# Optimization experiments

Hardware: AMD Instinct MI355X
Metric: run time of the kernel (lower is better)

Reference implementation:

```python
import jax, jax.numpy as jnp
import numpy as np

B, N, C_IN, C_OUT = 2, 512, 64, 64  # mid_dim == out_dim
EPS = 1e-5

def _bn(x, g, b):
    # PyTorch BatchNorm1d in training mode: biased batch stats over axis 0 of [M, C]
    mu = x.mean(axis=0)
    var = x.var(axis=0)
    return (x - mu) * jax.lax.rsqrt(var + EPS) * g + b

def setup_inputs() -> dict:
    key = jax.random.key(0)
    ks = jax.random.split(key, 16)
    s = 0.05
    return {
        "pos": jax.random.normal(ks[0], (B, N, 3), jnp.float32),
        "c_features": jax.random.normal(ks[1], (B, N, C_IN), jnp.float32),
        "Wq": jax.random.normal(ks[2], (C_OUT, C_IN), jnp.float32) * s,
        "bq": jnp.zeros((C_OUT,), jnp.float32),
        "Wk": jax.random.normal(ks[3], (C_OUT, C_IN), jnp.float32) * s,
        "bk": jnp.zeros((C_OUT,), jnp.float32),
        "Wv": jax.random.normal(ks[4], (C_OUT, C_IN), jnp.float32) * s,
        "bv": jnp.zeros((C_OUT,), jnp.float32),
        "Wp1": jax.random.normal(ks[5], (3, 3), jnp.float32) * s,
        "bp1": jnp.zeros((3,), jnp.float32),
        "g_p": jnp.ones((3,), jnp.float32),
        "b_p": jnp.zeros((3,), jnp.float32),
        "Wp2": jax.random.normal(ks[6], (C_OUT, 3), jnp.float32) * s,
        "bp2": jnp.zeros((C_OUT,), jnp.float32),
        "g_w": jnp.ones((C_OUT,), jnp.float32),
        "b_w": jnp.zeros((C_OUT,), jnp.float32),
        "Ww1": jax.random.normal(ks[7], (C_OUT, C_OUT), jnp.float32) * s,
        "bw1": jnp.zeros((C_OUT,), jnp.float32),
        "Ww2": jax.random.normal(ks[8], (C_OUT, C_OUT), jnp.float32) * s,
        "bw2": jnp.zeros((C_OUT,), jnp.float32),
    }

def reference(pos, c_features, Wq, bq, Wk, bk, Wv, bv, Wp1, bp1, g_p, b_p, Wp2, bp2, g_w, b_w, Ww1, bw1, Ww2, bw2):
    b, n = pos.shape[0], pos.shape[1]
    q = c_features @ Wq.T + bq                       # [B,N,Cmid]
    k = c_features @ Wk.T + bk
    v = c_features @ Wv.T + bv                       # [B,N,Cout]
    rel = pos[:, :, None, :] - pos[:, None, :, :]    # [B,N,N,3]
    h = rel.reshape(-1, 3) @ Wp1.T + bp1             # [B*N*N,3]
    h = jax.nn.relu(_bn(h, g_p, b_p))
    delta = (h @ Wp2.T + bp2).reshape(b, n, n, -1)   # [B,N,N,Cmid]
    qk = q[:, :, None, :] - k[:, None, :, :] + delta # [B,N,N,Cmid]
    h2 = _bn(qk.reshape(-1, qk.shape[-1]), g_w, b_w)
    h2 = jax.nn.relu(h2)
    h2 = jax.nn.relu(h2 @ Ww1.T + bw1)
    w = (h2 @ Ww2.T + bw2).reshape(b, n, n, -1)      # [B,N,N,Cout]
    attn = jax.nn.softmax(w, axis=2)                 # softmax over j
    out = jnp.sum(attn * (v[:, None, :, :] + delta), axis=2)  # [B,N,Cout]
    return out
```

## Files before the change

### kernel.cpp

```cpp
#include <hip/hip_runtime.h>
#include <stdint.h>
#include <stddef.h>

#define DEV __device__ __forceinline__

typedef __attribute__((ext_vector_type(4))) float f32x4;
typedef __attribute__((ext_vector_type(8))) short bf16x8;

union FragU { bf16x8 f; uint32_t u[4]; };

DEV uint32_t pk_bf16(float a, float b) {
  uint32_t d;
  asm("v_cvt_pk_bf16_f32 %0, %1, %2" : "=v"(d) : "v"(a), "v"(b));
  return d;
}

DEV uint16_t f2bf(float x) {
  uint32_t u = __float_as_uint(x);
  u += 0x7fffu + ((u >> 16) & 1u);
  return (uint16_t)(u >> 16);
}

__launch_bounds__(256)
__global__ void kP(const float* __restrict__ cf, const float* __restrict__ pos,
                   const float* __restrict__ Wq, const float* __restrict__ Wk,
                   const float* __restrict__ Wv, const float* __restrict__ bq,
                   const float* __restrict__ bk, const float* __restrict__ bv,
                   const float* __restrict__ Ww1, const float* __restrict__ Ww2,
                   const float* __restrict__ Wp1, const float* __restrict__ g_p,
                   const float* __restrict__ bp2,
                   float* __restrict__ qo, float* __restrict__ ko,
                   float* __restrict__ vT, uint16_t* __restrict__ W1bf,
                   uint16_t* __restrict__ W2bf, float* __restrict__ a1out,
                   unsigned int* __restrict__ counter) {
  const int bid = blockIdx.x, t = threadIdx.x;
  if (bid < 256) {
    __shared__ float cfl[4][64];
    const int rr = t >> 6, c = t & 63;
    const int r0 = bid * 4;
    cfl[rr][c] = cf[(size_t)(r0 + rr) * 64 + c];
    __syncthreads();
    const int bn = r0 + rr;
    const float* wqr = Wq + c * 64;
    const float* wkr = Wk + c * 64;
    const float* wvr = Wv + c * 64;
    float aq = bq[c], ak = bk[c], av = bv[c] + bp2[c];
#pragma unroll 8
    for (int kk = 0; kk < 64; ++kk) {
      const float f = cfl[rr][kk];
      aq = fmaf(f, wqr[kk], aq);
      ak = fmaf(f, wkr[kk], ak);
      av = fmaf(f, wvr[kk], av);
    }
    qo[(size_t)bn * 64 + c] = aq;
    ko[(size_t)bn * 64 + c] = ak;
    vT[((size_t)(bn >> 9) * 64 + c) * 512 + (bn & 511)] = av;
  } else if (bid == 256) {
    const float L2E = 1.4426950408889634f;
    for (int idx = t; idx < 8192; idx += 256) {
      const int m = idx >> 12;
      const int r = idx & 4095;
      const int f = r >> 9;
      const int l = (r >> 3) & 63;
      const int e = r & 7;
      const int nt = f >> 1, ks = f & 1, lm = l & 15, lq = l >> 4;
      const int row = 16 * nt + lm, col = 8 * lq + 32 * ks + e;
      const float src = m ? (Ww2[row * 64 + col] * L2E) : Ww1[row * 64 + col];
      (m ? W2bf : W1bf)[r] = f2bf(src);
    }
  } else {
    if (t == 0) counter[0] = 0u;
    __shared__ float acc9[2][9];
    __shared__ float red[256][10];
    __shared__ float red2[9][16];
    for (int b = 0; b < 2; ++b) {
      float s[9];
#pragma unroll
      for (int a = 0; a < 9; ++a) s[a] = 0.f;
      for (int r = 0; r < 2; ++r) {
        int i = t + 256 * r;
        const float* p = pos + (size_t)(b * 512 + i) * 3;
        float p0 = p[0], p1 = p[1], p2 = p[2];
        s[0] += p0; s[1] += p1; s[2] += p2;
        s[3] += p0 * p0; s[4] += p0 * p1; s[5] += p0 * p2;
        s[6] += p1 * p1; s[7] += p1 * p2; s[8] += p2 * p2;
      }
#pragma unroll
      for (int a = 0; a < 9; ++a) red[t][a] = s[a];
      __syncthreads();
      if (t < 144) {
        const int a = t >> 4, p = t & 15;
        float v = 0.f;
#pragma unroll
        for (int qq = 0; qq < 16; ++qq) v += red[p * 16 + qq][a];
        red2[a][p] = v;
      }
      __syncthreads();
      if (t < 9) {
        float v = 0.f;
#pragma unroll
        for (int p = 0; p < 16; ++p) v += red2[t][p];
        acc9[b][t] = v;
      }
      __syncthreads();
    }
    if (t == 0) {
      float C[6] = {0.f, 0.f, 0.f, 0.f, 0.f, 0.f};
      const float invM = 1.0f / 524288.0f;
      for (int b = 0; b < 2; ++b) {
        float S0 = acc9[b][0], S1 = acc9[b][1], S2 = acc9[b][2];
        float G00 = acc9[b][3], G01 = acc9[b][4], G02 = acc9[b][5];
        float G11 = acc9[b][6], G12 = acc9[b][7], G22 = acc9[b][8];
        C[0] += 1024.f * G00 - 2.f * S0 * S0;
        C[1] += 1024.f * G01 - 2.f * S0 * S1;
        C[2] += 1024.f * G02 - 2.f * S0 * S2;
        C[3] += 1024.f * G11 - 2.f * S1 * S1;
        C[4] += 1024.f * G12 - 2.f * S1 * S2;
        C[5] += 1024.f * G22 - 2.f * S2 * S2;
      }
      for (int a = 0; a < 6; ++a) C[a] *= invM;
      for (int tt = 0; tt < 3; ++tt) {
        float w0 = Wp1[tt * 3 + 0], w1 = Wp1[tt * 3 + 1], w2 = Wp1[tt * 3 + 2];
        float var = w0 * w0 * C[0] + w1 * w1 * C[3] + w2 * w2 * C[5]
                  + 2.f * (w0 * w1 * C[1] + w0 * w2 * C[2] + w1 * w2 * C[4]);
        a1out[tt] = g_p[tt] * rsqrtf(var + 1e-5f);
      }
      a1out[3] = 0.f;
    }
  }
}

__launch_bounds__(256)
__global__ void kB(const float* __restrict__ pos, const float* __restrict__ a1,
                   const float* __restrict__ Wp1, const float* __restrict__ b_p,
                   const float* __restrict__ q, const float* __restrict__ k,
                   const float* __restrict__ bp2,
                   const float* __restrict__ g_w, const float* __restrict__ b_w,
                   const float* __restrict__ Wp2,
                   float* __restrict__ hpa, float* __restrict__ Mpart,
                   float* __restrict__ XPp, float* __restrict__ SNp,
                   unsigned int* __restrict__ counter,
                   float* __restrict__ a2o, float* __restrict__ be2o,
                   float* __restrict__ PtT) {
  const int bid = blockIdx.x, t = threadIdx.x;
  const int s = bid >> 4, b = (bid >> 3) & 1, chunk = bid & 7;

  __shared__ __align__(16) f32x4 X[512];
  __shared__ float U[64][64];
  __shared__ float redr[64][4][4];
  __shared__ float mred[256][6];
  __shared__ float mred2[64][6];
  __shared__ float rfin[64][4];
  __shared__ float redn[256][2];
  __shared__ float MfS[6];
  __shared__ float ShfS[3];
  __shared__ unsigned int isLast;

  {
    const float a10 = a1[0], a11 = a1[1], a12 = a1[2];
    const float w00 = Wp1[0], w01 = Wp1[1], w02 = Wp1[2];
    const float w10 = Wp1[3], w11 = Wp1[4], w12 = Wp1[5];
    const float w20 = Wp1[6], w21 = Wp1[7], w22 = Wp1[8];
    for (int r = 0; r < 2; ++r) {
      const int row = t + 256 * r;
      const float* p = pos + (size_t)(b * 512 + row) * 3;
      const float p0 = p[0], p1 = p[1], p2 = p[2];
      f32x4 v;
      v.x = a10 * (w00 * p0 + w01 * p1 + w02 * p2);
      v.y = a11 * (w10 * p0 + w11 * p1 + w12 * p2);
      v.z = a12 * (w20 * p0 + w21 * p1 + w22 * p2);
      v.w = 0.f;
      if (s == 0 && chunk == 0)
        *(f32x4*)(hpa + (size_t)(b * 512 + row) * 4) = v;
      if (s) { v.x = -v.x; v.y = -v.y; v.z = -v.z; }
      X[row] = v;
    }
  }
  {
    const float* src = s ? k : q;
    const int r0g = b * 512 + chunk * 64;
#pragma unroll
    for (int e = 0; e < 16; ++e) {
      const int idx = e * 256 + t;
      const int row = idx >> 6, c = idx & 63;
      float v = src[(size_t)(r0g + row) * 64 + c];
      if (!s) v += bp2[c];
      U[row][c] = v;
    }
  }
  __syncthreads();

  {
    const int al = t >> 2, qr = t & 3;
    const int a = chunk * 64 + al;
    const f32x4 xa = X[a];
    const float base0 = xa.x + b_p[0], base1 = xa.y + b_p[1], base2 = xa.z + b_p[2];
    float r0 = 0, r1 = 0, r2 = 0;
    float m00 = 0, m01 = 0, m02 = 0, m11 = 0, m12 = 0, m22 = 0;
#pragma unroll 8
    for (int jj = qr * 128; jj < qr * 128 + 128; ++jj) {
      const f32x4 xj = X[jj];
      const float h0 = fmaxf(0.f, base0 - xj.x);
      const float h1 = fmaxf(0.f, base1 - xj.y);
      const float h2 = fmaxf(0.f, base2 - xj.z);
      r0 += h0; r1 += h1; r2 += h2;
      if (s == 0) {
        m00 = fmaf(h0, h0, m00); m01 = fmaf(h0, h1, m01); m02 = fmaf(h0, h2, m02);
        m11 = fmaf(h1, h1, m11); m12 = fmaf(h1, h2, m12); m22 = fmaf(h2, h2, m22);
      }
    }
    redr[al][qr][0] = r0; redr[al][qr][1] = r1; redr[al][qr][2] = r2; redr[al][qr][3] = 0.f;
    mred[t][0] = m00; mred[t][1] = m01; mred[t][2] = m02;
    mred[t][3] = m11; mred[t][4] = m12; mred[t][5] = m22;
  }
  __syncthreads();

  if (t < 64) {
    float sx = 0, sy = 0, sz = 0;
#pragma unroll
    for (int p = 0; p < 4; ++p) { sx += redr[t][p][0]; sy += redr[t][p][1]; sz += redr[t][p][2]; }
    rfin[t][0] = sx; rfin[t][1] = sy; rfin[t][2] = sz; rfin[t][3] = 0.f;
    if (s == 0) {
#pragma unroll
      for (int cc = 0; cc < 6; ++cc)
        mred2[t][cc] = mred[t][cc] + mred[t + 64][cc] + mred[t + 128][cc] + mred[t + 192][cc];
    }
  }
  __syncthreads();

  if (s == 0 && t < 6) {
    float m = 0.f;
    for (int p = 0; p < 64; ++p) m += mred2[p][t];
    Mpart[bid * 12 + t] = m;
  }
  if (s == 0 && t >= 64 && t < 67) {
    const int tt = t - 64;
    float v = 0.f;
#pragma unroll 8
    for (int a = 0; a < 64; ++a) v += rfin[a][tt];
    Mpart[bid * 12 + 6 + tt] = v;
  }
  if (t < 192) {
    const int c = t & 63, tt = t >> 6;
    float xp = 0.f;
#pragma unroll 8
    for (int a = 0; a < 64; ++a) xp = fmaf(U[a][c], rfin[a][tt], xp);
    if (s) xp = -xp;
    XPp[((size_t)bid * 3 + tt) * 64 + c] = xp;
  }
  {
    const int c = t & 63, g = t >> 6;
    float su = 0.f, su2 = 0.f;
#pragma unroll
    for (int r = 0; r < 16; ++r) {
      const float v = U[g * 16 + r][c];
      su += v;
      su2 = fmaf(v, v, su2);
    }
    redn[t][0] = su; redn[t][1] = su2;
  }
  __syncthreads();
  if (t < 64) {
    float a0 = 0.f, a1v = 0.f;
#pragma unroll
    for (int p = 0; p < 4; ++p) { a0 += redn[t + 64 * p][0]; a1v += redn[t + 64 * p][1]; }
    SNp[((size_t)bid * 2 + 0) * 64 + t] = a0;
    SNp[((size_t)bid * 2 + 1) * 64 + t] = a1v;
  }

  __syncthreads();
  if (t == 0) {
    __threadfence();
    const unsigned int old = atomicAdd(counter, 1u);
    isLast = (old == 31u) ? 1u : 0u;
  }
  __syncthreads();
  if (isLast) {
    __threadfence();
    if (t < 6) {
      float m = 0.f;
#pragma unroll
      for (int p = 0; p < 16; ++p) m += Mpart[p * 12 + t];
      MfS[t] = m;
    }
    if (t >= 6 && t < 9) {
      const int tt = t - 6;
      float v = 0.f;
#pragma unroll
      for (int p = 0; p < 16; ++p) v += Mpart[p * 12 + 6 + tt];
      ShfS[tt] = v;
    }
    __syncthreads();
    if (t < 64) {
      const int c = t;
      float Su[2], Su2[2], Sk[2], Sk2[2];
#pragma unroll
      for (int bb = 0; bb < 2; ++bb) {
        float a0 = 0.f, a1v = 0.f, a2v = 0.f, a3 = 0.f;
#pragma unroll
        for (int p = 0; p < 8; ++p) {
          const int blkU = bb * 8 + p;
          const int blkK = 16 + bb * 8 + p;
          a0 += SNp[((size_t)blkU * 2 + 0) * 64 + c];
          a1v += SNp[((size_t)blkU * 2 + 1) * 64 + c];
          a2v += SNp[((size_t)blkK * 2 + 0) * 64 + c];
          a3 += SNp[((size_t)blkK * 2 + 1) * 64 + c];
        }
        Su[bb] = a0; Su2[bb] = a1v; Sk[bb] = a2v; Sk2[bb] = a3;
      }
      float URd0 = 0.f, URd1 = 0.f, URd2 = 0.f;
#pragma unroll
      for (int blk = 0; blk < 32; ++blk) {
        URd0 += XPp[((size_t)blk * 3 + 0) * 64 + c];
        URd1 += XPp[((size_t)blk * 3 + 1) * 64 + c];
        URd2 += XPp[((size_t)blk * 3 + 2) * 64 + c];
      }
      const float P0t = Wp2[c * 3 + 0], P1t = Wp2[c * 3 + 1], P2t = Wp2[c * 3 + 2];
      const float Nf = 512.f, invM = 1.f / 524288.f;
      float S1 = 0.f, Q2 = 0.f;
#pragma unroll
      for (int bb = 0; bb < 2; ++bb) {
        S1 += Nf * (Su[bb] - Sk[bb]);
        Q2 += Nf * Su2[bb] - 2.f * Su[bb] * Sk[bb] + Nf * Sk2[bb];
      }
      const float Xc = P0t * URd0 + P1t * URd1 + P2t * URd2;
      S1 += P0t * ShfS[0] + P1t * ShfS[1] + P2t * ShfS[2];
      const float Hm = P0t * P0t * MfS[0] + 2.f * P0t * P1t * MfS[1] + 2.f * P0t * P2t * MfS[2]
                     + P1t * P1t * MfS[3] + 2.f * P1t * P2t * MfS[4] + P2t * P2t * MfS[5];
      const float E1 = S1 * invM;
      const float E2 = (Q2 + 2.f * Xc + Hm) * invM;
      const float var = E2 - E1 * E1;
      const float rstd = rsqrtf(var + 1e-5f);
      const float A2 = g_w[c] * rstd;
      a2o[c] = A2;
      be2o[c] = b_w[c] - E1 * A2;
      PtT[0 * 64 + c] = A2 * P0t;
      PtT[1 * 64 + c] = A2 * P1t;
      PtT[2 * 64 + c] = A2 * P2t;
    }
  }
}

__launch_bounds__(256)
__global__ void k3_main(const float* __restrict__ q, const float* __restrict__ kk_,
                        const float* __restrict__ vT, const float* __restrict__ hpa,
                        const float* __restrict__ a2g, const float* __restrict__ be2g,
                        const float* __restrict__ PtTg,
                        const uint16_t* __restrict__ W1bf, const uint16_t* __restrict__ W2bf,
                        const float* __restrict__ bp2, const float* __restrict__ Wp2,
                        const float* __restrict__ b_p, const float* __restrict__ bw1g,
                        const float* __restrict__ bw2g, float* __restrict__ out) {
  const int bid = blockIdx.x;
  const int b = bid >> 9, i = bid & 511;
  const int t = threadIdx.x;
  const int wid = t >> 6, l = t & 63;
  const int lm = l & 15, lq = l >> 4;

  __shared__ __align__(16) uint16_t W1l[4096];
  __shared__ __align__(16) uint16_t W2l[4096];
  __shared__ __align__(16) uint16_t H2[4][16][76];
  __shared__ __align__(16) float P0[64];
  __shared__ __align__(16) float a2s[64];
  __shared__ __align__(16) float Pts[3][64];
  __shared__ __align__(16) float comb[4][64][2];

  {
    *(bf16x8*)(&W1l[t * 16])     = *(const bf16x8*)(W1bf + t * 16);
    *(bf16x8*)(&W1l[t * 16 + 8]) = *(const bf16x8*)(W1bf + t * 16 + 8);
    *(bf16x8*)(&W2l[t * 16])     = *(const bf16x8*)(W2bf + t * 16);
    *(bf16x8*)(&W2l[t * 16 + 8]) = *(const bf16x8*)(W2bf + t * 16 + 8);
  }
  if (t < 64) {
    const float a2v = a2g[t];
    a2s[t] = a2v;
    P0[t] = fmaf(a2v, q[(size_t)(b * 512 + i) * 64 + t] + bp2[t], be2g[t]);
  } else {
    const int idx = t - 64;
    Pts[idx >> 6][idx & 63] = PtTg[idx];
  }

  const f32x4 hi = *(const f32x4*)(hpa + (size_t)(b * 512 + i) * 4);
  const float bb0 = b_p[0], bb1 = b_p[1], bb2 = b_p[2];
  const float LOG2E = 1.4426950408889634f;

  float bw1r[4], bw2l[4], wpa[4], wpb[4], wpc[4];
#pragma unroll
  for (int nt = 0; nt < 4; ++nt) {
    const int c = 16 * nt + lm;
    bw1r[nt] = bw1g[c];
    bw2l[nt] = bw2g[c] * LOG2E;
    wpa[nt] = Wp2[c * 3 + 0];
    wpb[nt] = Wp2[c * 3 + 1];
    wpc[nt] = Wp2[c * 3 + 2];
  }

  float l_[4] = {0.f, 0.f, 0.f, 0.f};
  float acc_[4] = {0.f, 0.f, 0.f, 0.f};

  __syncthreads();

  const float* kbase = kk_ + (size_t)(b * 512) * 64;
  const float* hbase = hpa + (size_t)(b * 512) * 4;
  const float* vTb = vT + (size_t)b * 64 * 512;

  f32x4 kvA[2][2];
  {
    const int j0 = wid * 16 + lm;
#pragma unroll
    for (int ks = 0; ks < 2; ++ks) {
      kvA[ks][0] = *(const f32x4*)(kbase + (size_t)j0 * 64 + 32 * ks + 8 * lq);
      kvA[ks][1] = *(const f32x4*)(kbase + (size_t)j0 * 64 + 32 * ks + 8 * lq + 4);
    }
  }

  for (int it = 0; it < 8; ++it) {
    const int jb = it * 64 + wid * 16;
    const int j = jb + lm;
    const int j2 = jb + 4 * lq;

    f32x4 kvN[2][2];
    if (it < 7) {
      const int jn = j + 64;
#pragma unroll
      for (int ks = 0; ks < 2; ++ks) {
        kvN[ks][0] = *(const f32x4*)(kbase + (size_t)jn * 64 + 32 * ks + 8 * lq);
        kvN[ks][1] = *(const f32x4*)(kbase + (size_t)jn * 64 + 32 * ks + 8 * lq + 4);
      }
    }

    const f32x4 hj = *(const f32x4*)(hbase + j * 4);
    f32x4 hjr[4];
#pragma unroll
    for (int r = 0; r < 4; ++r) hjr[r] = *(const f32x4*)(hbase + (j2 + r) * 4);
    f32x4 vv[4];
#pragma unroll
    for (int nt = 0; nt < 4; ++nt)
      vv[nt] = *(const f32x4*)(vTb + (size_t)(16 * nt + lm) * 512 + j2);

    const float h0 = fmaxf(0.f, hi.x - hj.x + bb0);
    const float h1 = fmaxf(0.f, hi.y - hj.y + bb1);
    const float h2v = fmaxf(0.f, hi.z - hj.z + bb2);

    FragU A1[2];
#pragma unroll
    for (int ks = 0; ks < 2; ++ks) {
      const int c0 = 32 * ks + 8 * lq;
      f32x4 pv[2], av[2], t0[2], t1[2], t2[2];
      pv[0] = *(const f32x4*)(P0 + c0);        pv[1] = *(const f32x4*)(P0 + c0 + 4);
      av[0] = *(const f32x4*)(a2s + c0);       av[1] = *(const f32x4*)(a2s + c0 + 4);
      t0[0] = *(const f32x4*)(&Pts[0][c0]);    t0[1] = *(const f32x4*)(&Pts[0][c0 + 4]);
      t1[0] = *(const f32x4*)(&Pts[1][c0]);    t1[1] = *(const f32x4*)(&Pts[1][c0 + 4]);
      t2[0] = *(const f32x4*)(&Pts[2][c0]);    t2[1] = *(const f32x4*)(&Pts[2][c0 + 4]);
      float x[8];
#pragma unroll
      for (int e = 0; e < 8; ++e) {
        const int hh = e >> 2, e4 = e & 3;
        float xv = pv[hh][e4] - av[hh][e4] * kvA[ks][hh][e4];
        xv = fmaf(t0[hh][e4], h0, xv);
        xv = fmaf(t1[hh][e4], h1, xv);
        xv = fmaf(t2[hh][e4], h2v, xv);
        x[e] = fmaxf(0.f, xv);
      }
      A1[ks].u[0] = pk_bf16(x[0], x[1]);
      A1[ks].u[1] = pk_bf16(x[2], x[3]);
      A1[ks].u[2] = pk_bf16(x[4], x[5]);
      A1[ks].u[3] = pk_bf16(x[6], x[7]);
    }

    f32x4 d1[4];
#pragma unroll
    for (int nt = 0; nt < 4; ++nt) {
      FragU b0, b1;
      b0.f = *(const bf16x8*)(&W1l[((nt * 2 + 0) * 64 + l) * 8]);
      b1.f = *(const bf16x8*)(&W1l[((nt * 2 + 1) * 64 + l) * 8]);
      f32x4 z = {bw1r[nt], bw1r[nt], bw1r[nt], bw1r[nt]};
      z = __builtin_amdgcn_mfma_f32_16x16x32_bf16(A1[0].f, b0.f, z, 0, 0, 0);
      z = __builtin_amdgcn_mfma_f32_16x16x32_bf16(A1[1].f, b1.f, z, 0, 0, 0);
      d1[nt] = z;
    }

    uint16_t (*h2w)[76] = H2[wid];
#pragma unroll
    for (int nt = 0; nt < 4; ++nt) {
      const uint32_t u01 = pk_bf16(fmaxf(0.f, d1[nt][0]), fmaxf(0.f, d1[nt][1]));
      const uint32_t u23 = pk_bf16(fmaxf(0.f, d1[nt][2]), fmaxf(0.f, d1[nt][3]));
      const int col = 16 * nt + lm;
      h2w[4 * lq + 0][col] = (uint16_t)(u01 & 0xffffu);
      h2w[4 * lq + 1][col] = (uint16_t)(u01 >> 16);
      h2w[4 * lq + 2][col] = (uint16_t)(u23 & 0xffffu);
      h2w[4 * lq + 3][col] = (uint16_t)(u23 >> 16);
    }

    FragU A2[2];
    A2[0].f = *(const bf16x8*)(&h2w[lm][8 * lq]);
    A2[1].f = *(const bf16x8*)(&h2w[lm][32 + 8 * lq]);

    f32x4 d2[4];
#pragma unroll
    for (int nt = 0; nt < 4; ++nt) {
      FragU b0, b1;
      b0.f = *(const bf16x8*)(&W2l[((nt * 2 + 0) * 64 + l) * 8]);
      b1.f = *(const bf16x8*)(&W2l[((nt * 2 + 1) * 64 + l) * 8]);
      f32x4 z = {bw2l[nt], bw2l[nt], bw2l[nt], bw2l[nt]};
      z = __builtin_amdgcn_mfma_f32_16x16x32_bf16(A2[0].f, b0.f, z, 0, 0, 0);
      z = __builtin_amdgcn_mfma_f32_16x16x32_bf16(A2[1].f, b1.f, z, 0, 0, 0);
      d2[nt] = z;
    }

    float hr0[4], hr1[4], hr2[4];
#pragma unroll
    for (int r = 0; r < 4; ++r) {
      hr0[r] = fmaxf(0.f, hi.x - hjr[r].x + bb0);
      hr1[r] = fmaxf(0.f, hi.y - hjr[r].y + bb1);
      hr2[r] = fmaxf(0.f, hi.z - hjr[r].z + bb2);
    }

#pragma unroll
    for (int nt = 0; nt < 4; ++nt) {
      float p[4], val[4];
#pragma unroll
      for (int r = 0; r < 4; ++r) {
        p[r] = __builtin_amdgcn_exp2f(d2[nt][r]);
        float v0 = vv[nt][r];
        v0 = fmaf(wpa[nt], hr0[r], v0);
        v0 = fmaf(wpb[nt], hr1[r], v0);
        v0 = fmaf(wpc[nt], hr2[r], v0);
        val[r] = v0;
      }
      l_[nt] += (p[0] + p[1]) + (p[2] + p[3]);
      float a = acc_[nt];
      a = fmaf(p[0], val[0], a);
      a = fmaf(p[1], val[1], a);
      a = fmaf(p[2], val[2], a);
      a = fmaf(p[3], val[3], a);
      acc_[nt] = a;
    }

    if (it < 7) {
#pragma unroll
      for (int ks = 0; ks < 2; ++ks) {
        kvA[ks][0] = kvN[ks][0];
        kvA[ks][1] = kvN[ks][1];
      }
    }
  }

#pragma unroll
  for (int nt = 0; nt < 4; ++nt) {
    l_[nt] += __shfl_xor(l_[nt], 16);
    acc_[nt] += __shfl_xor(acc_[nt], 16);
    l_[nt] += __shfl_xor(l_[nt], 32);
    acc_[nt] += __shfl_xor(acc_[nt], 32);
  }
  if (lq == 0) {
#pragma unroll
    for (int nt = 0; nt < 4; ++nt) {
      comb[wid][16 * nt + lm][0] = l_[nt];
      comb[wid][16 * nt + lm][1] = acc_[nt];
    }
  }
  __syncthreads();
  if (t < 64) {
    float L = 0.f, A = 0.f;
#pragma unroll
    for (int w = 0; w < 4; ++w) {
      L += comb[w][t][0];
      A += comb[w][t][1];
    }
    out[(size_t)(b * 512 + i) * 64 + t] = A / L;
  }
}

extern "C" void kernel_launch(void* const* d_in, const int* in_sizes, int n_in,
                              void* d_out, int out_size, void* d_ws, size_t ws_size,
                              hipStream_t stream) {
  (void)in_sizes; (void)n_in; (void)out_size; (void)ws_size;
  const float* pos = (const float*)d_in[0];
  const float* cf  = (const float*)d_in[1];
  const float* Wq  = (const float*)d_in[2];
  const float* bq  = (const float*)d_in[3];
  const float* Wk  = (const float*)d_in[4];
  const float* bk  = (const float*)d_in[5];
  const float* Wv  = (const float*)d_in[6];
  const float* bv  = (const float*)d_in[7];
  const float* Wp1 = (const float*)d_in[8];
  const float* g_p = (const float*)d_in[10];
  const float* b_p = (const float*)d_in[11];
  const float* Wp2 = (const float*)d_in[12];
  const float* bp2 = (const float*)d_in[13];
  const float* g_w = (const float*)d_in[14];
  const float* b_w = (const float*)d_in[15];
  const float* Ww1 = (const float*)d_in[16];
  const float* bw1 = (const float*)d_in[17];
  const float* Ww2 = (const float*)d_in[18];
  const float* bw2 = (const float*)d_in[19];

  char* ws = (char*)d_ws;
  uint16_t*     W1bf = (uint16_t*)(ws + 0);
  uint16_t*     W2bf = (uint16_t*)(ws + 8192);
  float*        a1w  = (float*)(ws + 16384);
  unsigned int* cnt  = (unsigned int*)(ws + 16640);
  float*        hpaw = (float*)(ws + 16896);
  float*        qw   = (float*)(ws + 33280);
  float*        kw   = (float*)(ws + 295424);
  float*        vTw  = (float*)(ws + 557568);
  float*        a2w  = (float*)(ws + 819712);
  float*        be2w = (float*)(ws + 819968);
  float*        PtTw = (float*)(ws + 820224);
  float*        Mpw  = (float*)(ws + 821248);
  float*        XPpw = (float*)(ws + 823040);
  float*        SNpw = (float*)(ws + 847872);

  kP<<<dim3(258), dim3(256), 0, stream>>>(cf, pos, Wq, Wk, Wv, bq, bk, bv,
                                          Ww1, Ww2, Wp1, g_p, bp2,
                                          qw, kw, vTw, W1bf, W2bf, a1w, cnt);
  kB<<<dim3(32), dim3(256), 0, stream>>>(pos, a1w, Wp1, b_p, qw, kw, bp2,
                                         g_w, b_w, Wp2,
                                         hpaw, Mpw, XPpw, SNpw, cnt,
                                         a2w, be2w, PtTw);
  k3_main<<<dim3(1024), dim3(256), 0, stream>>>(qw, kw, vTw, hpaw, a2w, be2w, PtTw,
                                                W1bf, W2bf, bp2, Wp2, b_p, bw1, bw2,
                                                (float*)d_out);
}
```

Before: 72.05 us.

## Merge prep kernels into one launch and finalize BN stats in main kernel

Folds the statistics kernel kB into the projection kernel as 32 extra blocks. These blocks recompute their own q/k tile from the raw features and compute the position BN scale locally, so they no longer wait on the earlier kernel's outputs. The last-block atomic reduction is removed, and each k3_main block now reduces the partial statistics itself to build the BN affine terms. This drops one kernel launch and the serial tail, at the cost of redundant per-block reduction work and duplicated q/k projection.

```diff
diff --git a/kernel.cpp b/kernel.cpp
--- a/kernel.cpp
+++ b/kernel.cpp
@@ -22,20 +22,32 @@
 }
 
 __launch_bounds__(256)
-__global__ void kP(const float* __restrict__ cf, const float* __restrict__ pos,
-                   const float* __restrict__ Wq, const float* __restrict__ Wk,
-                   const float* __restrict__ Wv, const float* __restrict__ bq,
-                   const float* __restrict__ bk, const float* __restrict__ bv,
-                   const float* __restrict__ Ww1, const float* __restrict__ Ww2,
-                   const float* __restrict__ Wp1, const float* __restrict__ g_p,
-                   const float* __restrict__ bp2,
-                   float* __restrict__ qo, float* __restrict__ ko,
-                   float* __restrict__ vT, uint16_t* __restrict__ W1bf,
-                   uint16_t* __restrict__ W2bf, float* __restrict__ a1out,
-                   unsigned int* __restrict__ counter) {
+__global__ void kAll(const float* __restrict__ cf, const float* __restrict__ pos,
+                     const float* __restrict__ Wq, const float* __restrict__ Wk,
+                     const float* __restrict__ Wv, const float* __restrict__ bq,
+                     const float* __restrict__ bk, const float* __restrict__ bv,
+                     const float* __restrict__ Ww1, const float* __restrict__ Ww2,
+                     const float* __restrict__ Wp1, const float* __restrict__ g_p,
+                     const float* __restrict__ b_p, const float* __restrict__ bp2,
+                     float* __restrict__ qo, float* __restrict__ ko,
+                     float* __restrict__ vT, uint16_t* __restrict__ W1bf,
+                     uint16_t* __restrict__ W2bf, float* __restrict__ hpa,
+                     float* __restrict__ Mpart, float* __restrict__ XPp,
+                     float* __restrict__ SNp) {
   const int bid = blockIdx.x, t = threadIdx.x;
+
+  __shared__ float cfl[4][64];
+  __shared__ __align__(16) f32x4 X[512];
+  __shared__ float U[64][64];
+  __shared__ float redr[64][4][4];
+  __shared__ float mred[256][6];
+  __shared__ float mred2[64][6];
+  __shared__ float rfin[64][4];
+  __shared__ float redn[256][2];
+  __shared__ float wred[4][2][9];
+  __shared__ float a1L[3];
+
   if (bid < 256) {
-    __shared__ float cfl[4][64];
     const int rr = t >> 6, c = t & 63;
     const int r0 = bid * 4;
     cfl[rr][c] = cf[(size_t)(r0 + rr) * 64 + c];
@@ -69,274 +81,182 @@
       (m ? W2bf : W1bf)[r] = f2bf(src);
     }
   } else {
-    if (t == 0) counter[0] = 0u;
-    __shared__ float acc9[2][9];
-    __shared__ float red[256][10];
-    __shared__ float red2[9][16];
-    for (int b = 0; b < 2; ++b) {
-      float s[9];
-#pragma unroll
-      for (int a = 0; a < 9; ++a) s[a] = 0.f;
-      for (int r = 0; r < 2; ++r) {
-        int i = t + 256 * r;
-        const float* p = pos + (size_t)(b * 512 + i) * 3;
-        float p0 = p[0], p1 = p[1], p2 = p[2];
-        s[0] += p0; s[1] += p1; s[2] += p2;
-        s[3] += p0 * p0; s[4] += p0 * p1; s[5] += p0 * p2;
-        s[6] += p1 * p1; s[7] += p1 * p2; s[8] += p2 * p2;
-      }
-#pragma unroll
-      for (int a = 0; a < 9; ++a) red[t][a] = s[a];
-      __syncthreads();
-      if (t < 144) {
-        const int a = t >> 4, p = t & 15;
-        float v = 0.f;
-#pragma unroll
-        for (int qq = 0; qq < 16; ++qq) v += red[p * 16 + qq][a];
-        red2[a][p] = v;
-      }
-      __syncthreads();
-      if (t < 9) {
-        float v = 0.f;
-#pragma unroll
-        for (int p = 0; p < 16; ++p) v += red2[t][p];
-        acc9[b][t] = v;
-      }
-      __syncthreads();
-    }
+    const int sb = bid - 257;
+    const int s = sb >> 4, b = (sb >> 3) & 1, chunk = sb & 7;
+    const int r0g = b * 512 + chunk * 64;
+
+    {
+      const int w = t >> 6, c = t & 63;
+      const float* wr = (s ? Wk : Wq) + c * 64;
+      const float bias = s ? bk[c] : (bq[c] + bp2[c]);
+      f32x4 wreg[16];
+#pragma unroll
+      for (int kv = 0; kv < 16; ++kv) wreg[kv] = *(const f32x4*)(wr + kv * 4);
+      for (int m = 0; m < 16; ++m) {
+        const int row = w * 16 + m;
+        const f32x4* cfr = (const f32x4*)(cf + (size_t)(r0g + row) * 64);
+        float a0 = bias, a1v = 0.f, a2v = 0.f, a3v = 0.f;
+#pragma unroll
+        for (int kv = 0; kv < 16; ++kv) {
+          const f32x4 f = cfr[kv];
+          a0 = fmaf(f.x, wreg[kv].x, a0);
+          a1v = fmaf(f.y, wreg[kv].y, a1v);
+          a2v = fmaf(f.z, wreg[kv].z, a2v);
+          a3v = fmaf(f.w, wreg[kv].w, a3v);
+        }
+        U[row][c] = (a0 + a1v) + (a2v + a3v);
+      }
+    }
+
+    {
+      const int l = t & 63, wid = t >> 6;
+      for (int b2 = 0; b2 < 2; ++b2) {
+        float s9[9] = {0, 0, 0, 0, 0, 0, 0, 0, 0};
+        for (int r = 0; r < 2; ++r) {
+          const int row = t + 256 * r;
+          const float* p = pos + (size_t)(b2 * 512 + row) * 3;
+          const float p0 = p[0], p1 = p[1], p2 = p[2];
+          s9[0] += p0; s9[1] += p1; s9[2] += p2;
+          s9[3] += p0 * p0; s9[4] += p0 * p1; s9[5] += p0 * p2;
+          s9[6] += p1 * p1; s9[7] += p1 * p2; s9[8] += p2 * p2;
+        }
+#pragma unroll
+        for (int a = 0; a < 9; ++a) {
+          float v = s9[a];
+          v += __shfl_xor(v, 1);  v += __shfl_xor(v, 2);  v += __shfl_xor(v, 4);
+          v += __shfl_xor(v, 8);  v += __shfl_xor(v, 16); v += __shfl_xor(v, 32);
+          s9[a] = v;
+        }
+        if (l == 0) {
+#pragma unroll
+          for (int a = 0; a < 9; ++a) wred[wid][b2][a] = s9[a];
+        }
+      }
+    }
+    __syncthreads();
     if (t == 0) {
-      float C[6] = {0.f, 0.f, 0.f, 0.f, 0.f, 0.f};
+      float C[6] = {0, 0, 0, 0, 0, 0};
       const float invM = 1.0f / 524288.0f;
-      for (int b = 0; b < 2; ++b) {
-        float S0 = acc9[b][0], S1 = acc9[b][1], S2 = acc9[b][2];
-        float G00 = acc9[b][3], G01 = acc9[b][4], G02 = acc9[b][5];
-        float G11 = acc9[b][6], G12 = acc9[b][7], G22 = acc9[b][8];
-        C[0] += 1024.f * G00 - 2.f * S0 * S0;
-        C[1] += 1024.f * G01 - 2.f * S0 * S1;
-        C[2] += 1024.f * G02 - 2.f * S0 * S2;
-        C[3] += 1024.f * G11 - 2.f * S1 * S1;
-        C[4] += 1024.f * G12 - 2.f * S1 * S2;
-        C[5] += 1024.f * G22 - 2.f * S2 * S2;
+      for (int b2 = 0; b2 < 2; ++b2) {
+        float acc9[9];
+#pragma unroll
+        for (int a = 0; a < 9; ++a)
+          acc9[a] = wred[0][b2][a] + wred[1][b2][a] + wred[2][b2][a] + wred[3][b2][a];
+        C[0] += 1024.f * acc9[3] - 2.f * acc9[0] * acc9[0];
+        C[1] += 1024.f * acc9[4] - 2.f * acc9[0] * acc9[1];
+        C[2] += 1024.f * acc9[5] - 2.f * acc9[0] * acc9[2];
+        C[3] += 1024.f * acc9[6] - 2.f * acc9[1] * acc9[1];
+        C[4] += 1024.f * acc9[7] - 2.f * acc9[1] * acc9[2];
+        C[5] += 1024.f * acc9[8] - 2.f * acc9[2] * acc9[2];
       }
       for (int a = 0; a < 6; ++a) C[a] *= invM;
       for (int tt = 0; tt < 3; ++tt) {
-        float w0 = Wp1[tt * 3 + 0], w1 = Wp1[tt * 3 + 1], w2 = Wp1[tt * 3 + 2];
-        float var = w0 * w0 * C[0] + w1 * w1 * C[3] + w2 * w2 * C[5]
-                  + 2.f * (w0 * w1 * C[1] + w0 * w2 * C[2] + w1 * w2 * C[4]);
-        a1out[tt] = g_p[tt] * rsqrtf(var + 1e-5f);
-      }
-      a1out[3] = 0.f;
-    }
-  }
-}
-
-__launch_bounds__(256)
-__global__ void kB(const float* __restrict__ pos, const float* __restrict__ a1,
-                   const float* __restrict__ Wp1, const float* __restrict__ b_p,
-                   const float* __restrict__ q, const float* __restrict__ k,
-                   const float* __restrict__ bp2,
-                   const float* __restrict__ g_w, const float* __restrict__ b_w,
-                   const float* __restrict__ Wp2,
-                   float* __restrict__ hpa, float* __restrict__ Mpart,
-                   float* __restrict__ XPp, float* __restrict__ SNp,
-                   unsigned int* __restrict__ counter,
-                   float* __restrict__ a2o, float* __restrict__ be2o,
-                   float* __restrict__ PtT) {
-  const int bid = blockIdx.x, t = threadIdx.x;
-  const int s = bid >> 4, b = (bid >> 3) & 1, chunk = bid & 7;
-
-  __shared__ __align__(16) f32x4 X[512];
-  __shared__ float U[64][64];
-  __shared__ float redr[64][4][4];
-  __shared__ float mred[256][6];
-  __shared__ float mred2[64][6];
-  __shared__ float rfin[64][4];
-  __shared__ float redn[256][2];
-  __shared__ float MfS[6];
-  __shared__ float ShfS[3];
-  __shared__ unsigned int isLast;
-
-  {
-    const float a10 = a1[0], a11 = a1[1], a12 = a1[2];
-    const float w00 = Wp1[0], w01 = Wp1[1], w02 = Wp1[2];
-    const float w10 = Wp1[3], w11 = Wp1[4], w12 = Wp1[5];
-    const float w20 = Wp1[6], w21 = Wp1[7], w22 = Wp1[8];
-    for (int r = 0; r < 2; ++r) {
-      const int row = t + 256 * r;
-      const float* p = pos + (size_t)(b * 512 + row) * 3;
-      const float p0 = p[0], p1 = p[1], p2 = p[2];
-      f32x4 v;
-      v.x = a10 * (w00 * p0 + w01 * p1 + w02 * p2);
-      v.y = a11 * (w10 * p0 + w11 * p1 + w12 * p2);
-      v.z = a12 * (w20 * p0 + w21 * p1 + w22 * p2);
-      v.w = 0.f;
-      if (s == 0 && chunk == 0)
-        *(f32x4*)(hpa + (size_t)(b * 512 + row) * 4) = v;
-      if (s) { v.x = -v.x; v.y = -v.y; v.z = -v.z; }
-      X[row] = v;
-    }
-  }
-  {
-    const float* src = s ? k : q;
-    const int r0g = b * 512 + chunk * 64;
-#pragma unroll
-    for (int e = 0; e < 16; ++e) {
-      const int idx = e * 256 + t;
-      const int row = idx >> 6, c = idx & 63;
-      float v = src[(size_t)(r0g + row) * 64 + c];
-      if (!s) v += bp2[c];
-      U[row][c] = v;
-    }
-  }
-  __syncthreads();
-
-  {
-    const int al = t >> 2, qr = t & 3;
-    const int a = chunk * 64 + al;
-    const f32x4 xa = X[a];
-    const float base0 = xa.x + b_p[0], base1 = xa.y + b_p[1], base2 = xa.z + b_p[2];
-    float r0 = 0, r1 = 0, r2 = 0;
-    float m00 = 0, m01 = 0, m02 = 0, m11 = 0, m12 = 0, m22 = 0;
+        const float w0 = Wp1[tt * 3 + 0], w1 = Wp1[tt * 3 + 1], w2 = Wp1[tt * 3 + 2];
+        const float var = w0 * w0 * C[0] + w1 * w1 * C[3] + w2 * w2 * C[5]
+                        + 2.f * (w0 * w1 * C[1] + w0 * w2 * C[2] + w1 * w2 * C[4]);
+        a1L[tt] = g_p[tt] * rsqrtf(var + 1e-5f);
+      }
+    }
+    __syncthreads();
+
+    {
+      const float a10 = a1L[0], a11 = a1L[1], a12 = a1L[2];
+      const float w00 = Wp1[0], w01 = Wp1[1], w02 = Wp1[2];
+      const float w10 = Wp1[3], w11 = Wp1[4], w12 = Wp1[5];
+      const float w20 = Wp1[6], w21 = Wp1[7], w22 = Wp1[8];
+      for (int r = 0; r < 2; ++r) {
+        const int row = t + 256 * r;
+        const float* p = pos + (size_t)(b * 512 + row) * 3;
+        const float p0 = p[0], p1 = p[1], p2 = p[2];
+        f32x4 v;
+        v.x = a10 * (w00 * p0 + w01 * p1 + w02 * p2);
+        v.y = a11 * (w10 * p0 + w11 * p1 + w12 * p2);
+        v.z = a12 * (w20 * p0 + w21 * p1 + w22 * p2);
+        v.w = 0.f;
+        if (s == 0 && chunk == 0)
+          *(f32x4*)(hpa + (size_t)(b * 512 + row) * 4) = v;
+        if (s) { v.x = -v.x; v.y = -v.y; v.z = -v.z; }
+        X[row] = v;
+      }
+    }
+    __syncthreads();
+
+    {
+      const int al = t >> 2, qr = t & 3;
+      const int a = chunk * 64 + al;
+      const f32x4 xa = X[a];
+      const float base0 = xa.x + b_p[0], base1 = xa.y + b_p[1], base2 = xa.z + b_p[2];
+      float r0 = 0, r1 = 0, r2 = 0;
+      float m00 = 0, m01 = 0, m02 = 0, m11 = 0, m12 = 0, m22 = 0;
 #pragma unroll 8
-    for (int jj = qr * 128; jj < qr * 128 + 128; ++jj) {
-      const f32x4 xj = X[jj];
-      const float h0 = fmaxf(0.f, base0 - xj.x);
-      const float h1 = fmaxf(0.f, base1 - xj.y);
-      const float h2 = fmaxf(0.f, base2 - xj.z);
-      r0 += h0; r1 += h1; r2 += h2;
+      for (int jj = qr * 128; jj < qr * 128 + 128; ++jj) {
+        const f32x4 xj = X[jj];
+        const float h0 = fmaxf(0.f, base0 - xj.x);
+        const float h1 = fmaxf(0.f, base1 - xj.y);
+        const float h2 = fmaxf(0.f, base2 - xj.z);
+        r0 += h0; r1 += h1; r2 += h2;
+        if (s == 0) {
+          m00 = fmaf(h0, h0, m00); m01 = fmaf(h0, h1, m01); m02 = fmaf(h0, h2, m02);
+          m11 = fmaf(h1, h1, m11); m12 = fmaf(h1, h2, m12); m22 = fmaf(h2, h2, m22);
+        }
+      }
+      redr[al][qr][0] = r0; redr[al][qr][1] = r1; redr[al][qr][2] = r2; redr[al][qr][3] = 0.f;
+      mred[t][0] = m00; mred[t][1] = m01; mred[t][2] = m02;
+      mred[t][3] = m11; mred[t][4] = m12; mred[t][5] = m22;
+    }
+    __syncthreads();
+
+    if (t < 64) {
+      float sx = 0, sy = 0, sz = 0;
+#pragma unroll
+      for (int p = 0; p < 4; ++p) { sx += redr[t][p][0]; sy += redr[t][p][1]; sz += redr[t][p][2]; }
+      rfin[t][0] = sx; rfin[t][1] = sy; rfin[t][2] = sz; rfin[t][3] = 0.f;
       if (s == 0) {
-        m00 = fmaf(h0, h0, m00); m01 = fmaf(h0, h1, m01); m02 = fmaf(h0, h2, m02);
-        m11 = fmaf(h1, h1, m11); m12 = fmaf(h1, h2, m12); m22 = fmaf(h2, h2, m22);
-      }
-    }
-    redr[al][qr][0] = r0; redr[al][qr][1] = r1; redr[al][qr][2] = r2; redr[al][qr][3] = 0.f;
-    mred[t][0] = m00; mred[t][1] = m01; mred[t][2] = m02;
-    mred[t][3] = m11; mred[t][4] = m12; mred[t][5] = m22;
-  }
-  __syncthreads();
-
-  if (t < 64) {
-    float sx = 0, sy = 0, sz = 0;
-#pragma unroll
-    for (int p = 0; p < 4; ++p) { sx += redr[t][p][0]; sy += redr[t][p][1]; sz += redr[t][p][2]; }
-    rfin[t][0] = sx; rfin[t][1] = sy; rfin[t][2] = sz; rfin[t][3] = 0.f;
-    if (s == 0) {
-#pragma unroll
-      for (int cc = 0; cc < 6; ++cc)
-        mred2[t][cc] = mred[t][cc] + mred[t + 64][cc] + mred[t + 128][cc] + mred[t + 192][cc];
-    }
-  }
-  __syncthreads();
-
-  if (s == 0 && t < 6) {
-    float m = 0.f;
-    for (int p = 0; p < 64; ++p) m += mred2[p][t];
-    Mpart[bid * 12 + t] = m;
-  }
-  if (s == 0 && t >= 64 && t < 67) {
-    const int tt = t - 64;
-    float v = 0.f;
+#pragma unroll
+        for (int cc = 0; cc < 6; ++cc)
+          mred2[t][cc] = mred[t][cc] + mred[t + 64][cc] + mred[t + 128][cc] + mred[t + 192][cc];
+      }
+    }
+    __syncthreads();
+
+    if (s == 0 && t < 6) {
+      float m = 0.f;
+      for (int p = 0; p < 64; ++p) m += mred2[p][t];
+      Mpart[sb * 12 + t] = m;
+    }
+    if (s == 0 && t >= 64 && t < 67) {
+      const int tt = t - 64;
+      float v = 0.f;
 #pragma unroll 8
-    for (int a = 0; a < 64; ++a) v += rfin[a][tt];
-    Mpart[bid * 12 + 6 + tt] = v;
-  }
-  if (t < 192) {
-    const int c = t & 63, tt = t >> 6;
-    float xp = 0.f;
+      for (int a = 0; a < 64; ++a) v += rfin[a][tt];
+      Mpart[sb * 12 + 6 + tt] = v;
+    }
+    if (t < 192) {
+      const int c = t & 63, tt = t >> 6;
+      float xp = 0.f;
 #pragma unroll 8
-    for (int a = 0; a < 64; ++a) xp = fmaf(U[a][c], rfin[a][tt], xp);
-    if (s) xp = -xp;
-    XPp[((size_t)bid * 3 + tt) * 64 + c] = xp;
-  }
-  {
-    const int c = t & 63, g = t >> 6;
-    float su = 0.f, su2 = 0.f;
-#pragma unroll
-    for (int r = 0; r < 16; ++r) {
-      const float v = U[g * 16 + r][c];
-      su += v;
-      su2 = fmaf(v, v, su2);
-    }
-    redn[t][0] = su; redn[t][1] = su2;
-  }
-  __syncthreads();
-  if (t < 64) {
-    float a0 = 0.f, a1v = 0.f;
-#pragma unroll
-    for (int p = 0; p < 4; ++p) { a0 += redn[t + 64 * p][0]; a1v += redn[t + 64 * p][1]; }
-    SNp[((size_t)bid * 2 + 0) * 64 + t] = a0;
-    SNp[((size_t)bid * 2 + 1) * 64 + t] = a1v;
-  }
-
-  __syncthreads();
-  if (t == 0) {
-    __threadfence();
-    const unsigned int old = atomicAdd(counter, 1u);
-    isLast = (old == 31u) ? 1u : 0u;
-  }
-  __syncthreads();
-  if (isLast) {
-    __threadfence();
-    if (t < 6) {
-      float m = 0.f;
-#pragma unroll
-      for (int p = 0; p < 16; ++p) m += Mpart[p * 12 + t];
-      MfS[t] = m;
-    }
-    if (t >= 6 && t < 9) {
-      const int tt = t - 6;
-      float v = 0.f;
-#pragma unroll
-      for (int p = 0; p < 16; ++p) v += Mpart[p * 12 + 6 + tt];
-      ShfS[tt] = v;
+      for (int a = 0; a < 64; ++a) xp = fmaf(U[a][c], rfin[a][tt], xp);
+      if (s) xp = -xp;
+      XPp[((size_t)sb * 3 + tt) * 64 + c] = xp;
+    }
+    {
+      const int c = t & 63, g = t >> 6;
+      float su = 0.f, su2 = 0.f;
+#pragma unroll
+      for (int r = 0; r < 16; ++r) {
+        const float v = U[g * 16 + r][c];
+        su += v;
+        su2 = fmaf(v, v, su2);
+      }
+      redn[t][0] = su; redn[t][1] = su2;
     }
     __syncthreads();
     if (t < 64) {
-      const int c = t;
-      float Su[2], Su2[2], Sk[2], Sk2[2];
-#pragma unroll
-      for (int bb = 0; bb < 2; ++bb) {
-        float a0 = 0.f, a1v = 0.f, a2v = 0.f, a3 = 0.f;
-#pragma unroll
-        for (int p = 0; p < 8; ++p) {
-          const int blkU = bb * 8 + p;
-          const int blkK = 16 + bb * 8 + p;
-          a0 += SNp[((size_t)blkU * 2 + 0) * 64 + c];
-          a1v += SNp[((size_t)blkU * 2 + 1) * 64 + c];
-          a2v += SNp[((size_t)blkK * 2 + 0) * 64 + c];
-          a3 += SNp[((size_t)blkK * 2 + 1) * 64 + c];
-        }
-        Su[bb] = a0; Su2[bb] = a1v; Sk[bb] = a2v; Sk2[bb] = a3;
-      }
-      float URd0 = 0.f, URd1 = 0.f, URd2 = 0.f;
-#pragma unroll
-      for (int blk = 0; blk < 32; ++blk) {
-        URd0 += XPp[((size_t)blk * 3 + 0) * 64 + c];
-        URd1 += XPp[((size_t)blk * 3 + 1) * 64 + c];
-        URd2 += XPp[((size_t)blk * 3 + 2) * 64 + c];
-      }
-      const float P0t = Wp2[c * 3 + 0], P1t = Wp2[c * 3 + 1], P2t = Wp2[c * 3 + 2];
-      const float Nf = 512.f, invM = 1.f / 524288.f;
-      float S1 = 0.f, Q2 = 0.f;
-#pragma unroll
-      for (int bb = 0; bb < 2; ++bb) {
-        S1 += Nf * (Su[bb] - Sk[bb]);
-        Q2 += Nf * Su2[bb] - 2.f * Su[bb] * Sk[bb] + Nf * Sk2[bb];
-      }
-      const float Xc = P0t * URd0 + P1t * URd1 + P2t * URd2;
-      S1 += P0t * ShfS[0] + P1t * ShfS[1] + P2t * ShfS[2];
-      const float Hm = P0t * P0t * MfS[0] + 2.f * P0t * P1t * MfS[1] + 2.f * P0t * P2t * MfS[2]
-                     + P1t * P1t * MfS[3] + 2.f * P1t * P2t * MfS[4] + P2t * P2t * MfS[5];
-      const float E1 = S1 * invM;
-      const float E2 = (Q2 + 2.f * Xc + Hm) * invM;
-      const float var = E2 - E1 * E1;
-      const float rstd = rsqrtf(var + 1e-5f);
-      const float A2 = g_w[c] * rstd;
-      a2o[c] = A2;
-      be2o[c] = b_w[c] - E1 * A2;
-      PtT[0 * 64 + c] = A2 * P0t;
-      PtT[1 * 64 + c] = A2 * P1t;
-      PtT[2 * 64 + c] = A2 * P2t;
+      float a0 = 0.f, a1v = 0.f;
+#pragma unroll
+      for (int p = 0; p < 4; ++p) { a0 += redn[t + 64 * p][0]; a1v += redn[t + 64 * p][1]; }
+      SNp[((size_t)sb * 2 + 0) * 64 + t] = a0;
+      SNp[((size_t)sb * 2 + 1) * 64 + t] = a1v;
     }
   }
 }
@@ -344,8 +264,9 @@
 __launch_bounds__(256)
 __global__ void k3_main(const float* __restrict__ q, const float* __restrict__ kk_,
                         const float* __restrict__ vT, const float* __restrict__ hpa,
-                        const float* __restrict__ a2g, const float* __restrict__ be2g,
-                        const float* __restrict__ PtTg,
+                        const float* __restrict__ Mpart, const float* __restrict__ XPp,
+                        const float* __restrict__ SNp, const float* __restrict__ g_w,
+                        const float* __restrict__ b_w,
                         const uint16_t* __restrict__ W1bf, const uint16_t* __restrict__ W2bf,
                         const float* __restrict__ bp2, const float* __restrict__ Wp2,
                         const float* __restrict__ b_p, const float* __restrict__ bw1g,
@@ -363,6 +284,9 @@
   __shared__ __align__(16) float a2s[64];
   __shared__ __align__(16) float Pts[3][64];
   __shared__ __align__(16) float comb[4][64][2];
+  __shared__ float xps[4][3][64];
+  __shared__ float sns[4][2][64];
+  __shared__ float msh[12];
 
   {
     *(bf16x8*)(&W1l[t * 16])     = *(const bf16x8*)(W1bf + t * 16);
@@ -370,13 +294,58 @@
     *(bf16x8*)(&W2l[t * 16])     = *(const bf16x8*)(W2bf + t * 16);
     *(bf16x8*)(&W2l[t * 16 + 8]) = *(const bf16x8*)(W2bf + t * 16 + 8);
   }
+
+  {
+    const int qd = t >> 6, c = t & 63;
+    float x0 = 0, x1 = 0, x2 = 0, s0 = 0, s1 = 0;
+#pragma unroll
+    for (int p = 0; p < 8; ++p) {
+      const int blk = qd * 8 + p;
+      x0 += XPp[((size_t)blk * 3 + 0) * 64 + c];
+      x1 += XPp[((size_t)blk * 3 + 1) * 64 + c];
+      x2 += XPp[((size_t)blk * 3 + 2) * 64 + c];
+      s0 += SNp[((size_t)blk * 2 + 0) * 64 + c];
+      s1 += SNp[((size_t)blk * 2 + 1) * 64 + c];
+    }
+    xps[qd][0][c] = x0; xps[qd][1][c] = x1; xps[qd][2][c] = x2;
+    sns[qd][0][c] = s0; sns[qd][1][c] = s1;
+    if (t < 12) {
+      float m = 0.f;
+#pragma unroll
+      for (int p = 0; p < 16; ++p) m += Mpart[p * 12 + t];
+      msh[t] = m;
+    }
+  }
+  __syncthreads();
+
   if (t < 64) {
-    const float a2v = a2g[t];
-    a2s[t] = a2v;
-    P0[t] = fmaf(a2v, q[(size_t)(b * 512 + i) * 64 + t] + bp2[t], be2g[t]);
-  } else {
-    const int idx = t - 64;
-    Pts[idx >> 6][idx & 63] = PtTg[idx];
+    const int c = t;
+    const float URd0 = xps[0][0][c] + xps[1][0][c] + xps[2][0][c] + xps[3][0][c];
+    const float URd1 = xps[0][1][c] + xps[1][1][c] + xps[2][1][c] + xps[3][1][c];
+    const float URd2 = xps[0][2][c] + xps[1][2][c] + xps[2][2][c] + xps[3][2][c];
+    const float Su0 = sns[0][0][c], Su20 = sns[0][1][c];
+    const float Su1 = sns[1][0][c], Su21 = sns[1][1][c];
+    const float Sk0 = sns[2][0][c], Sk20 = sns[2][1][c];
+    const float Sk1 = sns[3][0][c], Sk21 = sns[3][1][c];
+    const float P0t = Wp2[c * 3 + 0], P1t = Wp2[c * 3 + 1], P2t = Wp2[c * 3 + 2];
+    const float Nf = 512.f, invM = 1.f / 524288.f;
+    float S1 = Nf * (Su0 - Sk0) + Nf * (Su1 - Sk1);
+    const float Q2 = Nf * Su20 - 2.f * Su0 * Sk0 + Nf * Sk20
+                   + Nf * Su21 - 2.f * Su1 * Sk1 + Nf * Sk21;
+    const float Xc = P0t * URd0 + P1t * URd1 + P2t * URd2;
+    S1 += P0t * msh[6] + P1t * msh[7] + P2t * msh[8];
+    const float Hm = P0t * P0t * msh[0] + 2.f * P0t * P1t * msh[1] + 2.f * P0t * P2t * msh[2]
+                   + P1t * P1t * msh[3] + 2.f * P1t * P2t * msh[4] + P2t * P2t * msh[5];
+    const float E1 = S1 * invM;
+    const float E2 = (Q2 + 2.f * Xc + Hm) * invM;
+    const float var = E2 - E1 * E1;
+    const float A2 = g_w[c] * rsqrtf(var + 1e-5f);
+    const float be2 = b_w[c] - E1 * A2;
+    a2s[c] = A2;
+    P0[c] = fmaf(A2, q[(size_t)(b * 512 + i) * 64 + c] + bp2[c], be2);
+    Pts[0][c] = A2 * P0t;
+    Pts[1][c] = A2 * P1t;
+    Pts[2][c] = A2 * P2t;
   }
 
   const f32x4 hi = *(const f32x4*)(hpa + (size_t)(b * 512 + i) * 4);
@@ -596,29 +565,21 @@
   const float* bw2 = (const float*)d_in[19];
 
   char* ws = (char*)d_ws;
-  uint16_t*     W1bf = (uint16_t*)(ws + 0);
-  uint16_t*     W2bf = (uint16_t*)(ws + 8192);
-  float*        a1w  = (float*)(ws + 16384);
-  unsigned int* cnt  = (unsigned int*)(ws + 16640);
-  float*        hpaw = (float*)(ws + 16896);
-  float*        qw   = (float*)(ws + 33280);
-  float*        kw   = (float*)(ws + 295424);
-  float*        vTw  = (float*)(ws + 557568);
-  float*        a2w  = (float*)(ws + 819712);
-  float*        be2w = (float*)(ws + 819968);
-  float*        PtTw = (float*)(ws + 820224);
-  float*        Mpw  = (float*)(ws + 821248);
-  float*        XPpw = (float*)(ws + 823040);
-  float*        SNpw = (float*)(ws + 847872);
-
-  kP<<<dim3(258), dim3(256), 0, stream>>>(cf, pos, Wq, Wk, Wv, bq, bk, bv,
-                                          Ww1, Ww2, Wp1, g_p, bp2,
-                                          qw, kw, vTw, W1bf, W2bf, a1w, cnt);
-  kB<<<dim3(32), dim3(256), 0, stream>>>(pos, a1w, Wp1, b_p, qw, kw, bp2,
-                                         g_w, b_w, Wp2,
-                                         hpaw, Mpw, XPpw, SNpw, cnt,
-                                         a2w, be2w, PtTw);
-  k3_main<<<dim3(1024), dim3(256), 0, stream>>>(qw, kw, vTw, hpaw, a2w, be2w, PtTw,
-                                                W1bf, W2bf, bp2, Wp2, b_p, bw1, bw2,
-                                                (float*)d_out);
+  uint16_t* W1bf = (uint16_t*)(ws + 0);
+  uint16_t* W2bf = (uint16_t*)(ws + 8192);
+  float*    hpaw = (float*)(ws + 16896);
+  float*    qw   = (float*)(ws + 33280);
+  float*    kw   = (float*)(ws + 295424);
+  float*    vTw  = (float*)(ws + 557568);
+  float*    Mpw  = (float*)(ws + 821248);
+  float*    XPpw = (float*)(ws + 823040);
+  float*    SNpw = (float*)(ws + 847872);
+
+  kAll<<<dim3(289), dim3(256), 0, stream>>>(cf, pos, Wq, Wk, Wv, bq, bk, bv,
+                                            Ww1, Ww2, Wp1, g_p, b_p, bp2,
+                                            qw, kw, vTw, W1bf, W2bf, hpaw,
+                                            Mpw, XPpw, SNpw);
+  k3_main<<<dim3(1024), dim3(256), 0, stream>>>(qw, kw, vTw, hpaw, Mpw, XPpw, SNpw,
+                                                g_w, b_w, W1bf, W2bf, bp2, Wp2, b_p,
+                                                bw1, bw2, (float*)d_out);
 }
```

After: 74.53 us. +3.4%, slower.
